# Optimization experiments

Hardware: AMD Instinct MI355X
Metric: run time of the kernel (lower is better)

Reference implementation:

```python
import jax, jax.numpy as jnp
import numpy as np

B, N, D = 4, 4096, 1024


def setup_inputs() -> dict:
    key = jax.random.key(0)
    ks = jax.random.split(key, 7)
    s = 1.0 / np.sqrt(D)
    return {
        "x": jax.random.normal(ks[0], (B, N, D), dtype=jnp.float32),
        "Wq": jax.random.uniform(ks[1], (D, D), jnp.float32, -s, s),
        "bq": jax.random.uniform(ks[2], (D,), jnp.float32, -s, s),
        "Wk": jax.random.uniform(ks[3], (D, D), jnp.float32, -s, s),
        "bk": jax.random.uniform(ks[4], (D,), jnp.float32, -s, s),
        "Wv": jax.random.uniform(ks[5], (D, D), jnp.float32, -s, s),
        "bv": jax.random.uniform(ks[6], (D,), jnp.float32, -s, s),
    }


def reference(x, Wq, bq, Wk, bk, Wv, bv):
    # Projections (nn.Linear: x @ W.T + b; here W stored as [in, out])
    Q = x @ Wq + bq
    K = x @ Wk + bk
    V = x @ Wv + bv
    Qp = jax.nn.elu(Q) + 1.0  # positive feature map
    Kp = jax.nn.elu(K) + 1.0
    KV = jnp.einsum('bnd,bne->bde', Kp, V)          # [B, D, D]
    numerator = jnp.einsum('bnd,bde->bne', Qp, KV)  # [B, N, D]
    K_sum = Kp.sum(axis=1)                           # [B, D]
    norm = jnp.einsum('bnd,bd->bn', Qp, K_sum)[..., None]
    eps = 1e-6
    return numerator / (norm + eps)
```

## Files before the change

kernel.cpp:

```cpp
#include <hip/hip_runtime.h>
#include <hip/hip_bf16.h>
#include <cstdint>

typedef __bf16 bf16x8 __attribute__((ext_vector_type(8)));
typedef float  f32x4  __attribute__((ext_vector_type(4)));
typedef unsigned short u16x8 __attribute__((ext_vector_type(8)));

__device__ __forceinline__ unsigned short f2bf(float f) {
  __hip_bfloat16 h = __float2bfloat16(f);
  return __builtin_bit_cast(unsigned short, h);
}
__device__ __forceinline__ float bf2f(unsigned short u) {
  return __builtin_bit_cast(float, (unsigned)u << 16);
}

#define GL2LDS16(gp, lp)                                                      \
  __builtin_amdgcn_global_load_lds(                                           \
      (const __attribute__((address_space(1))) unsigned int*)(gp),            \
      (__attribute__((address_space(3))) unsigned int*)(lp), 16, 0, 0)

#define SBAR                                                                  \
  {                                                                           \
    __builtin_amdgcn_s_barrier();                                             \
    __builtin_amdgcn_sched_barrier(0);                                        \
  }
#define WAITV(n)                                                              \
  {                                                                           \
    asm volatile("s_waitcnt vmcnt(" #n ")" ::: "memory");                     \
    __builtin_amdgcn_sched_barrier(0);                                        \
  }
#define WAITL0                                                                \
  {                                                                           \
    asm volatile("s_waitcnt lgkmcnt(0)" ::: "memory");                        \
    __builtin_amdgcn_sched_barrier(0);                                        \
  }

template <int MODE>
__global__ __launch_bounds__(512, 2) void gemm256(
    const unsigned short* __restrict__ A, long long lda, long long aOffZ,
    const unsigned short* __restrict__ B, long long ldb, long long bOffZ,
    void* __restrict__ C, long long ldc, long long cOffZ,
    const float* __restrict__ bias, const float* __restrict__ bias2,
    const float* __restrict__ norm, long long normOffZ, int K) {
  __shared__ __attribute__((aligned(16))) char lds[4 * 32768];
  const int t = threadIdx.x;
  const int wave = t >> 6, lane = t & 63;
  const int wm = wave >> 2, wn = wave & 3;
  const int fr = lane & 15, fq = lane >> 4;

  const int gx = gridDim.x, gy = gridDim.y;
  int flat = blockIdx.y * gx + blockIdx.x;
  const int total = gx * gy;
  if ((total & 7) == 0) flat = (flat & 7) * (total >> 3) + (flat >> 3);
  int bx, by;
  if (MODE == 1) {
    bx = flat / gy;
    by = flat - bx * gy;
  } else {
    bx = flat % gx;
    by = flat / gx;
  }
  const int m0 = by * 256, n0 = bx * 256;

  const long long z = blockIdx.z;
  long long aBase, bBase;
  if (MODE == 3) {
    const long long koff = (z & 3) * 4096 + (z >> 2) * 1024;
    aBase = koff;
    bBase = koff;
  } else {
    aBase = z * aOffZ;
    bBase = z * bOffZ;
  }
  const unsigned short* Az = A + aBase;
  const unsigned short* Bz = B + bBase;

  const unsigned short* gA[2];
  const unsigned short* gB[2];
#pragma unroll
  for (int c = 0; c < 2; ++c) {
    int d = c * 8192 + t * 16;
    int l = d ^ (((d >> 7) & 3) << 4);
    int row = l >> 6, kel = (l & 63) >> 1;
    gA[c] = Az + (long long)(m0 + row) * lda + kel;
    gB[c] = Bz + (long long)(n0 + row) * ldb + kel;
  }

  const int slotx = (fr >> 1) & 3;
  const int abase = wm * 8192 + fr * 64 + ((fq ^ slotx) << 4);
  const int bbase = 16384 + wn * 4096 + fr * 64 + ((fq ^ slotx) << 4);

  f32x4 acc[8][4];
#pragma unroll
  for (int i = 0; i < 8; ++i)
#pragma unroll
    for (int j = 0; j < 4; ++j) acc[i][j] = (f32x4){0.f, 0.f, 0.f, 0.f};

  const int NT = K >> 5;

  auto stage = [&](int tile) {
    const int k0 = tile << 5;
    char* bufp = lds + (tile & 3) * 32768;
#pragma unroll
    for (int c = 0; c < 2; ++c)
      GL2LDS16(gA[c] + k0, bufp + c * 8192 + wave * 1024);
#pragma unroll
    for (int c = 0; c < 2; ++c)
      GL2LDS16(gB[c] + k0, bufp + 16384 + c * 8192 + wave * 1024);
  };

  stage(0);
  stage(1);
  stage(2);
  WAITV(8);
  SBAR;

  bf16x8 av[8], bv[4];
  for (int tt = 0; tt < NT - 3; ++tt) {
    const char* bufp = lds + (tt & 3) * 32768;
    stage(tt + 3);
#pragma unroll
    for (int i = 0; i < 4; ++i) {
      av[i] = *(const bf16x8*)(bufp + abase + i * 1024);
      av[4 + i] = *(const bf16x8*)(bufp + abase + 4096 + i * 1024);
      bv[i] = *(const bf16x8*)(bufp + bbase + i * 1024);
    }
    WAITL0;
    __builtin_amdgcn_s_setprio(1);
#pragma unroll
    for (int mi = 0; mi < 8; ++mi)
#pragma unroll
      for (int ni = 0; ni < 4; ++ni)
        acc[mi][ni] = __builtin_amdgcn_mfma_f32_16x16x32_bf16(
            av[mi], bv[ni], acc[mi][ni], 0, 0, 0);
    __builtin_amdgcn_s_setprio(0);
    WAITV(8);
    SBAR;
  }

  WAITV(0);
  SBAR;
#pragma unroll
  for (int e = 0; e < 3; ++e) {
    const char* bufp = lds + ((NT - 3 + e) & 3) * 32768;
#pragma unroll
    for (int i = 0; i < 4; ++i) {
      av[i] = *(const bf16x8*)(bufp + abase + i * 1024);
      av[4 + i] = *(const bf16x8*)(bufp + abase + 4096 + i * 1024);
      bv[i] = *(const bf16x8*)(bufp + bbase + i * 1024);
    }
#pragma unroll
    for (int mi = 0; mi < 8; ++mi)
#pragma unroll
      for (int ni = 0; ni < 4; ++ni)
        acc[mi][ni] = __builtin_amdgcn_mfma_f32_16x16x32_bf16(
            av[mi], bv[ni], acc[mi][ni], 0, 0, 0);
  }

  const float* nrmz = (MODE == 4) ? (norm + z * normOffZ) : nullptr;
  float* Cf = (float*)C + z * cOffZ;
  unsigned short* Cu = (unsigned short*)C + z * cOffZ;
  const bool lower = (m0 < 1024);
#pragma unroll
  for (int mi = 0; mi < 8; ++mi) {
    const int rbase = m0 + wm * 128 + mi * 16 + fq * 4;
    float rb[4], nv[4];
#pragma unroll
    for (int j = 0; j < 4; ++j) {
      if (MODE == 1)
        rb[j] = lower ? bias[rbase + j] : bias2[rbase - 1024 + j];
      if (MODE == 4) nv[j] = nrmz[rbase + j];
    }
#pragma unroll
    for (int ni = 0; ni < 4; ++ni) {
      const int c = n0 + wn * 64 + ni * 16 + fr;
      float cb = 0.f;
      if (MODE == 0) cb = bias[c];
#pragma unroll
      for (int j = 0; j < 4; ++j) {
        float v = acc[mi][ni][j];
        if (MODE == 0) v += cb;
        if (MODE == 1) v += rb[j];
        if (MODE == 0 || (MODE == 1 && lower))
          v = (v > 0.f) ? v + 1.f : __expf(v);
        const long long ci = (long long)(rbase + j) * ldc + c;
        if (MODE == 4)
          Cf[ci] = v / nv[j];
        else
          Cu[ci] = f2bf(v);
      }
    }
  }
}

__global__ __launch_bounds__(256) void reduce_kvt(
    const unsigned short* __restrict__ P, unsigned short* __restrict__ KVt) {
  const long long i = ((long long)blockIdx.x * 256 + threadIdx.x) * 8;
  const int b = (int)(i >> 20);
  const long long ed = i & ((1ll << 20) - 1);
  float s[8] = {0.f, 0.f, 0.f, 0.f, 0.f, 0.f, 0.f, 0.f};
#pragma unroll
  for (int ks = 0; ks < 4; ++ks) {
    u16x8 v = *(const u16x8*)(P + ((long long)(ks * 4 + b) << 20) + ed);
#pragma unroll
    for (int j = 0; j < 8; ++j) s[j] += bf2f(v[j]);
  }
  u16x8 o;
#pragma unroll
  for (int j = 0; j < 8; ++j) o[j] = f2bf(s[j]);
  *(u16x8*)(KVt + i) = o;
}

__global__ __launch_bounds__(256) void transpose_w(
    const float* __restrict__ W, unsigned short* __restrict__ WT) {
  __shared__ float tile[32][33];
  const int tx = threadIdx.x & 31, ty = threadIdx.x >> 5;
  const int i0 = blockIdx.y * 32, o0 = blockIdx.x * 32;
#pragma unroll
  for (int s = 0; s < 32; s += 8)
    tile[ty + s][tx] = W[(long long)(i0 + ty + s) * 1024 + o0 + tx];
  __syncthreads();
#pragma unroll
  for (int s = 0; s < 32; s += 8)
    WT[(long long)(o0 + ty + s) * 1024 + i0 + tx] = f2bf(tile[tx][ty + s]);
}

__global__ __launch_bounds__(256) void convert_x(
    const float4* __restrict__ in, uint2* __restrict__ out, int n4) {
  const int stride = gridDim.x * blockDim.x;
  for (int i = blockIdx.x * blockDim.x + threadIdx.x; i < n4; i += stride) {
    float4 v = in[i];
    uint2 o;
    o.x = (unsigned)f2bf(v.x) | ((unsigned)f2bf(v.y) << 16);
    o.y = (unsigned)f2bf(v.z) | ((unsigned)f2bf(v.w) << 16);
    out[i] = o;
  }
}

__global__ __launch_bounds__(256) void ksum_kernel(
    const unsigned short* __restrict__ KpT, float* __restrict__ Ksum) {
  const int gw = (blockIdx.x * 256 + threadIdx.x) >> 6;
  const int lane = threadIdx.x & 63;
  const int d = gw >> 2, b = gw & 3;
  const unsigned short* p = KpT + (long long)d * 16384 + b * 4096 + lane * 8;
  float s = 0.f;
#pragma unroll
  for (int it = 0; it < 8; ++it) {
    u16x8 v = *(const u16x8*)(p + it * 512);
#pragma unroll
    for (int j = 0; j < 8; ++j) s += bf2f(v[j]);
  }
#pragma unroll
  for (int o = 32; o > 0; o >>= 1) s += __shfl_down(s, o, 64);
  if (lane == 0) Ksum[b * 1024 + d] = s;
}

__global__ __launch_bounds__(256) void norm_kernel(
    const unsigned short* __restrict__ Qp, const float* __restrict__ Ksum,
    float* __restrict__ nrm) {
  const int gw = (blockIdx.x * 256 + threadIdx.x) >> 6;
  const int lane = threadIdx.x & 63;
  const int b = gw >> 12;
  const unsigned short* q = Qp + (long long)gw * 1024 + lane * 8;
  const float* ks = Ksum + b * 1024 + lane * 8;
  float s = 0.f;
#pragma unroll
  for (int it = 0; it < 2; ++it) {
    u16x8 v = *(const u16x8*)(q + it * 512);
    float4 k0 = *(const float4*)(ks + it * 512);
    float4 k1 = *(const float4*)(ks + it * 512 + 4);
    s += bf2f(v[0]) * k0.x + bf2f(v[1]) * k0.y + bf2f(v[2]) * k0.z +
         bf2f(v[3]) * k0.w + bf2f(v[4]) * k1.x + bf2f(v[5]) * k1.y +
         bf2f(v[6]) * k1.z + bf2f(v[7]) * k1.w;
  }
#pragma unroll
  for (int o = 32; o > 0; o >>= 1) s += __shfl_down(s, o, 64);
  if (lane == 0) nrm[gw] = s + 1e-6f;
}

extern "C" void kernel_launch(void* const* d_in, const int* in_sizes, int n_in,
                              void* d_out, int out_size, void* d_ws,
                              size_t ws_size, hipStream_t stream) {
  const float* x  = (const float*)d_in[0];
  const float* Wq = (const float*)d_in[1];
  const float* bq = (const float*)d_in[2];
  const float* Wk = (const float*)d_in[3];
  const float* bk = (const float*)d_in[4];
  const float* Wv = (const float*)d_in[5];
  const float* bv = (const float*)d_in[6];
  float* out = (float*)d_out;

  const size_t MN = 16384ull * 1024ull;
  char* w = (char*)d_ws;
  unsigned short* xb  = (unsigned short*)w;  w += MN * 2;
  unsigned short* WT  = (unsigned short*)w;  w += 3ull * 1024 * 1024 * 2;
  unsigned short* Qp  = (unsigned short*)w;  w += MN * 2;
  unsigned short* KVb = (unsigned short*)w;  w += 2 * MN * 2;
  unsigned short* KVt = (unsigned short*)w;  w += 4ull * 1024 * 1024 * 2;
  float* Ksum = (float*)w;  w += 4ull * 1024 * 4;
  float* nrm  = (float*)w;  w += 16384ull * 4;
  unsigned short* Pkv = xb;
  unsigned short* KpT = KVb;
  unsigned short* VT  = KVb + MN;

  transpose_w<<<dim3(32, 32), 256, 0, stream>>>(Wq, WT);
  transpose_w<<<dim3(32, 32), 256, 0, stream>>>(Wk, WT + 1024 * 1024);
  transpose_w<<<dim3(32, 32), 256, 0, stream>>>(Wv, WT + 2 * 1024 * 1024);
  convert_x<<<2048, 256, 0, stream>>>((const float4*)x, (uint2*)xb,
                                      (int)(MN / 4));

  gemm256<0><<<dim3(4, 64, 1), 512, 0, stream>>>(
      xb, 1024, 0, WT, 1024, 0, Qp, 1024, 0, bq, nullptr, nullptr, 0, 1024);
  gemm256<1><<<dim3(64, 8, 1), 512, 0, stream>>>(
      WT + 1024 * 1024, 1024, 0, xb, 1024, 0, KVb, 16384, 0, bk, bv, nullptr,
      0, 1024);
  ksum_kernel<<<1024, 256, 0, stream>>>(KpT, Ksum);
  gemm256<3><<<dim3(4, 4, 16), 512, 0, stream>>>(
      VT, 16384, 0, KpT, 16384, 0, Pkv, 1024, 1024 * 1024, nullptr, nullptr,
      nullptr, 0, 1024);
  reduce_kvt<<<2048, 256, 0, stream>>>(Pkv, KVt);
  norm_kernel<<<4096, 256, 0, stream>>>(Qp, Ksum, nrm);
  gemm256<4><<<dim3(4, 16, 4), 512, 0, stream>>>(
      Qp, 1024, 4096ll * 1024, KVt, 1024, 1024 * 1024, out, 1024,
      4096ll * 1024, nullptr, nullptr, nrm, 4096, 1024);
}
```

Before: 254.8 us.

## Restructure GEMM main loop into double-buffered 64-wide K tiles with sub-stage interleaving

Replaces the 4-deep ring of 32-wide K tiles with two 64 KB buffers, each holding a 64-wide K tile. Each iteration is split into four sub-phases that interleave LDS fragment reads, quarter-tile global-to-LDS prefetches for the next tile, and half-sized MFMA blocks. The aim is to lower register pressure (av shrinks from 8 to 4 vectors) and spread load issue across the compute. In exchange it adds many more barriers per K step and cuts prefetch depth to one tile ahead, which may expose memory latency.

```diff
diff --git a/kernel.cpp b/kernel.cpp
--- a/kernel.cpp
+++ b/kernel.cpp
@@ -42,7 +42,7 @@
     void* __restrict__ C, long long ldc, long long cOffZ,
     const float* __restrict__ bias, const float* __restrict__ bias2,
     const float* __restrict__ norm, long long normOffZ, int K) {
-  __shared__ __attribute__((aligned(16))) char lds[4 * 32768];
+  __shared__ __attribute__((aligned(16))) char lds[2 * 65536];
   const int t = threadIdx.x;
   const int wave = t >> 6, lane = t & 63;
   const int wm = wave >> 2, wn = wave & 3;
@@ -87,8 +87,8 @@
   }
 
   const int slotx = (fr >> 1) & 3;
-  const int abase = wm * 8192 + fr * 64 + ((fq ^ slotx) << 4);
-  const int bbase = 16384 + wn * 4096 + fr * 64 + ((fq ^ slotx) << 4);
+  const int acore = wm * 8192 + fr * 64 + ((fq ^ slotx) << 4);
+  const int bcore = wn * 4096 + fr * 64 + ((fq ^ slotx) << 4);
 
   f32x4 acc[8][4];
 #pragma unroll
@@ -96,65 +96,149 @@
 #pragma unroll
     for (int j = 0; j < 4; ++j) acc[i][j] = (f32x4){0.f, 0.f, 0.f, 0.f};
 
-  const int NT = K >> 5;
-
-  auto stage = [&](int tile) {
-    const int k0 = tile << 5;
-    char* bufp = lds + (tile & 3) * 32768;
-#pragma unroll
-    for (int c = 0; c < 2; ++c)
-      GL2LDS16(gA[c] + k0, bufp + c * 8192 + wave * 1024);
-#pragma unroll
-    for (int c = 0; c < 2; ++c)
-      GL2LDS16(gB[c] + k0, bufp + 16384 + c * 8192 + wave * 1024);
+  const int NT = K >> 6;
+
+  auto stage_sub = [&](int tile, int which) {
+    char* dst = lds + (tile & 1) * 65536 + which * 16384 + wave * 1024;
+    const int kofs = (tile << 6) + ((which >> 1) << 5);
+    if (which & 1) {
+      GL2LDS16(gB[0] + kofs, dst);
+      GL2LDS16(gB[1] + kofs, dst + 8192);
+    } else {
+      GL2LDS16(gA[0] + kofs, dst);
+      GL2LDS16(gA[1] + kofs, dst + 8192);
+    }
   };
 
-  stage(0);
-  stage(1);
-  stage(2);
-  WAITV(8);
+  stage_sub(0, 0);
+  stage_sub(0, 1);
+  stage_sub(0, 2);
+  stage_sub(0, 3);
+  WAITV(4);
   SBAR;
 
-  bf16x8 av[8], bv[4];
-  for (int tt = 0; tt < NT - 3; ++tt) {
-    const char* bufp = lds + (tt & 3) * 32768;
-    stage(tt + 3);
+  bf16x8 av[4], bv0[4], bv1[4];
+  for (int tt = 0; tt < NT - 1; ++tt) {
+    const char* bufp = lds + (tt & 1) * 65536;
 #pragma unroll
     for (int i = 0; i < 4; ++i) {
-      av[i] = *(const bf16x8*)(bufp + abase + i * 1024);
-      av[4 + i] = *(const bf16x8*)(bufp + abase + 4096 + i * 1024);
-      bv[i] = *(const bf16x8*)(bufp + bbase + i * 1024);
-    }
+      av[i] = *(const bf16x8*)(bufp + acore + i * 1024);
+      bv0[i] = *(const bf16x8*)(bufp + 16384 + bcore + i * 1024);
+    }
+    stage_sub(tt + 1, 0);
+    SBAR;
     WAITL0;
     __builtin_amdgcn_s_setprio(1);
 #pragma unroll
-    for (int mi = 0; mi < 8; ++mi)
+    for (int mi = 0; mi < 4; ++mi)
 #pragma unroll
       for (int ni = 0; ni < 4; ++ni)
         acc[mi][ni] = __builtin_amdgcn_mfma_f32_16x16x32_bf16(
-            av[mi], bv[ni], acc[mi][ni], 0, 0, 0);
+            av[mi], bv0[ni], acc[mi][ni], 0, 0, 0);
     __builtin_amdgcn_s_setprio(0);
-    WAITV(8);
-    SBAR;
-  }
-
-  WAITV(0);
-  SBAR;
-#pragma unroll
-  for (int e = 0; e < 3; ++e) {
-    const char* bufp = lds + ((NT - 3 + e) & 3) * 32768;
+    SBAR;
+#pragma unroll
+    for (int i = 0; i < 4; ++i)
+      av[i] = *(const bf16x8*)(bufp + acore + (4 + i) * 1024);
+    stage_sub(tt + 1, 1);
+    SBAR;
+    WAITL0;
+    __builtin_amdgcn_s_setprio(1);
+#pragma unroll
+    for (int mi = 0; mi < 4; ++mi)
+#pragma unroll
+      for (int ni = 0; ni < 4; ++ni)
+        acc[4 + mi][ni] = __builtin_amdgcn_mfma_f32_16x16x32_bf16(
+            av[mi], bv0[ni], acc[4 + mi][ni], 0, 0, 0);
+    __builtin_amdgcn_s_setprio(0);
+    WAITV(4);
+    SBAR;
 #pragma unroll
     for (int i = 0; i < 4; ++i) {
-      av[i] = *(const bf16x8*)(bufp + abase + i * 1024);
-      av[4 + i] = *(const bf16x8*)(bufp + abase + 4096 + i * 1024);
-      bv[i] = *(const bf16x8*)(bufp + bbase + i * 1024);
-    }
-#pragma unroll
-    for (int mi = 0; mi < 8; ++mi)
+      av[i] = *(const bf16x8*)(bufp + 32768 + acore + i * 1024);
+      bv1[i] = *(const bf16x8*)(bufp + 49152 + bcore + i * 1024);
+    }
+    stage_sub(tt + 1, 2);
+    SBAR;
+    WAITL0;
+    __builtin_amdgcn_s_setprio(1);
+#pragma unroll
+    for (int mi = 0; mi < 4; ++mi)
 #pragma unroll
       for (int ni = 0; ni < 4; ++ni)
         acc[mi][ni] = __builtin_amdgcn_mfma_f32_16x16x32_bf16(
-            av[mi], bv[ni], acc[mi][ni], 0, 0, 0);
+            av[mi], bv1[ni], acc[mi][ni], 0, 0, 0);
+    __builtin_amdgcn_s_setprio(0);
+    SBAR;
+#pragma unroll
+    for (int i = 0; i < 4; ++i)
+      av[i] = *(const bf16x8*)(bufp + 32768 + acore + (4 + i) * 1024);
+    stage_sub(tt + 1, 3);
+    SBAR;
+    WAITL0;
+    __builtin_amdgcn_s_setprio(1);
+#pragma unroll
+    for (int mi = 0; mi < 4; ++mi)
+#pragma unroll
+      for (int ni = 0; ni < 4; ++ni)
+        acc[4 + mi][ni] = __builtin_amdgcn_mfma_f32_16x16x32_bf16(
+            av[mi], bv1[ni], acc[4 + mi][ni], 0, 0, 0);
+    __builtin_amdgcn_s_setprio(0);
+    WAITV(4);
+    SBAR;
+  }
+
+  {
+    const char* bufp = lds + ((NT - 1) & 1) * 65536;
+#pragma unroll
+    for (int i = 0; i < 4; ++i) {
+      av[i] = *(const bf16x8*)(bufp + acore + i * 1024);
+      bv0[i] = *(const bf16x8*)(bufp + 16384 + bcore + i * 1024);
+    }
+    SBAR;
+    WAITL0;
+#pragma unroll
+    for (int mi = 0; mi < 4; ++mi)
+#pragma unroll
+      for (int ni = 0; ni < 4; ++ni)
+        acc[mi][ni] = __builtin_amdgcn_mfma_f32_16x16x32_bf16(
+            av[mi], bv0[ni], acc[mi][ni], 0, 0, 0);
+    SBAR;
+#pragma unroll
+    for (int i = 0; i < 4; ++i)
+      av[i] = *(const bf16x8*)(bufp + acore + (4 + i) * 1024);
+    SBAR;
+    WAITL0;
+#pragma unroll
+    for (int mi = 0; mi < 4; ++mi)
+#pragma unroll
+      for (int ni = 0; ni < 4; ++ni)
+        acc[4 + mi][ni] = __builtin_amdgcn_mfma_f32_16x16x32_bf16(
+            av[mi], bv0[ni], acc[4 + mi][ni], 0, 0, 0);
+    WAITV(0);
+    SBAR;
+#pragma unroll
+    for (int i = 0; i < 4; ++i) {
+      av[i] = *(const bf16x8*)(bufp + 32768 + acore + i * 1024);
+      bv1[i] = *(const bf16x8*)(bufp + 49152 + bcore + i * 1024);
+    }
+    WAITL0;
+#pragma unroll
+    for (int mi = 0; mi < 4; ++mi)
+#pragma unroll
+      for (int ni = 0; ni < 4; ++ni)
+        acc[mi][ni] = __builtin_amdgcn_mfma_f32_16x16x32_bf16(
+            av[mi], bv1[ni], acc[mi][ni], 0, 0, 0);
+#pragma unroll
+    for (int i = 0; i < 4; ++i)
+      av[i] = *(const bf16x8*)(bufp + 32768 + acore + (4 + i) * 1024);
+    WAITL0;
+#pragma unroll
+    for (int mi = 0; mi < 4; ++mi)
+#pragma unroll
+      for (int ni = 0; ni < 4; ++ni)
+        acc[4 + mi][ni] = __builtin_amdgcn_mfma_f32_16x16x32_bf16(
+            av[mi], bv1[ni], acc[4 + mi][ni], 0, 0, 0);
   }
 
   const float* nrmz = (MODE == 4) ? (norm + z * normOffZ) : nullptr;
```

Measured after the change: 250.9 us. About the same (-1.5%).

## Use 1024-thread blocks with 16 waves and triple-buffered LDS in GEMMs

Applied to the files above, without the earlier changes.

The GEMM kernel now launches 1024 threads (16 waves in a 4x4 grid), and each wave computes a 64x64 sub-tile instead of 128x64. The block tile stays 256x256. Per-wave accumulators and A fragments are halved, each thread issues one global-to-LDS load per operand, and the LDS pipeline drops from 4 stages to 3 (96 KB). The aim is more waves in flight per CU to hide latency, at the cost of less register reuse per LDS read and a shallower prefetch depth.

```diff
diff --git a/kernel.cpp b/kernel.cpp
--- a/kernel.cpp
+++ b/kernel.cpp
@@ -36,13 +36,13 @@
   }
 
 template <int MODE>
-__global__ __launch_bounds__(512, 2) void gemm256(
+__global__ __launch_bounds__(1024, 4) void gemm256w(
     const unsigned short* __restrict__ A, long long lda, long long aOffZ,
     const unsigned short* __restrict__ B, long long ldb, long long bOffZ,
     void* __restrict__ C, long long ldc, long long cOffZ,
     const float* __restrict__ bias, const float* __restrict__ bias2,
     const float* __restrict__ norm, long long normOffZ, int K) {
-  __shared__ __attribute__((aligned(16))) char lds[4 * 32768];
+  __shared__ __attribute__((aligned(16))) char lds[3 * 32768];
   const int t = threadIdx.x;
   const int wave = t >> 6, lane = t & 63;
   const int wm = wave >> 2, wn = wave & 3;
@@ -75,82 +75,89 @@
   const unsigned short* Az = A + aBase;
   const unsigned short* Bz = B + bBase;
 
-  const unsigned short* gA[2];
-  const unsigned short* gB[2];
-#pragma unroll
-  for (int c = 0; c < 2; ++c) {
-    int d = c * 8192 + t * 16;
+  const unsigned short* gA;
+  const unsigned short* gB;
+  {
+    int d = t * 16;
     int l = d ^ (((d >> 7) & 3) << 4);
     int row = l >> 6, kel = (l & 63) >> 1;
-    gA[c] = Az + (long long)(m0 + row) * lda + kel;
-    gB[c] = Bz + (long long)(n0 + row) * ldb + kel;
+    gA = Az + (long long)(m0 + row) * lda + kel;
+    gB = Bz + (long long)(n0 + row) * ldb + kel;
   }
 
   const int slotx = (fr >> 1) & 3;
-  const int abase = wm * 8192 + fr * 64 + ((fq ^ slotx) << 4);
-  const int bbase = 16384 + wn * 4096 + fr * 64 + ((fq ^ slotx) << 4);
-
-  f32x4 acc[8][4];
-#pragma unroll
-  for (int i = 0; i < 8; ++i)
+  const int acore = wm * 4096 + fr * 64 + ((fq ^ slotx) << 4);
+  const int bcore = 16384 + wn * 4096 + fr * 64 + ((fq ^ slotx) << 4);
+
+  f32x4 acc[4][4];
+#pragma unroll
+  for (int i = 0; i < 4; ++i)
 #pragma unroll
     for (int j = 0; j < 4; ++j) acc[i][j] = (f32x4){0.f, 0.f, 0.f, 0.f};
 
   const int NT = K >> 5;
 
   auto stage = [&](int tile) {
+    char* sb = lds + (tile % 3) * 32768 + wave * 1024;
     const int k0 = tile << 5;
-    char* bufp = lds + (tile & 3) * 32768;
-#pragma unroll
-    for (int c = 0; c < 2; ++c)
-      GL2LDS16(gA[c] + k0, bufp + c * 8192 + wave * 1024);
-#pragma unroll
-    for (int c = 0; c < 2; ++c)
-      GL2LDS16(gB[c] + k0, bufp + 16384 + c * 8192 + wave * 1024);
+    GL2LDS16(gA + k0, sb);
+    GL2LDS16(gB + k0, sb + 16384);
   };
 
   stage(0);
   stage(1);
-  stage(2);
-  WAITV(8);
+  WAITV(2);
   SBAR;
 
-  bf16x8 av[8], bv[4];
-  for (int tt = 0; tt < NT - 3; ++tt) {
-    const char* bufp = lds + (tt & 3) * 32768;
-    stage(tt + 3);
+  bf16x8 av[4], bv[4];
+  for (int tt = 0; tt < NT - 2; ++tt) {
+    const char* sb = lds + (tt % 3) * 32768;
+    stage(tt + 2);
 #pragma unroll
     for (int i = 0; i < 4; ++i) {
-      av[i] = *(const bf16x8*)(bufp + abase + i * 1024);
-      av[4 + i] = *(const bf16x8*)(bufp + abase + 4096 + i * 1024);
-      bv[i] = *(const bf16x8*)(bufp + bbase + i * 1024);
+      av[i] = *(const bf16x8*)(sb + acore + i * 1024);
+      bv[i] = *(const bf16x8*)(sb + bcore + i * 1024);
     }
     WAITL0;
     __builtin_amdgcn_s_setprio(1);
 #pragma unroll
-    for (int mi = 0; mi < 8; ++mi)
+    for (int mi = 0; mi < 4; ++mi)
 #pragma unroll
       for (int ni = 0; ni < 4; ++ni)
         acc[mi][ni] = __builtin_amdgcn_mfma_f32_16x16x32_bf16(
             av[mi], bv[ni], acc[mi][ni], 0, 0, 0);
     __builtin_amdgcn_s_setprio(0);
-    WAITV(8);
+    WAITV(2);
     SBAR;
   }
 
-  WAITV(0);
-  SBAR;
-#pragma unroll
-  for (int e = 0; e < 3; ++e) {
-    const char* bufp = lds + ((NT - 3 + e) & 3) * 32768;
+  {
+    const char* sb = lds + ((NT - 2) % 3) * 32768;
 #pragma unroll
     for (int i = 0; i < 4; ++i) {
-      av[i] = *(const bf16x8*)(bufp + abase + i * 1024);
-      av[4 + i] = *(const bf16x8*)(bufp + abase + 4096 + i * 1024);
-      bv[i] = *(const bf16x8*)(bufp + bbase + i * 1024);
-    }
-#pragma unroll
-    for (int mi = 0; mi < 8; ++mi)
+      av[i] = *(const bf16x8*)(sb + acore + i * 1024);
+      bv[i] = *(const bf16x8*)(sb + bcore + i * 1024);
+    }
+    WAITL0;
+#pragma unroll
+    for (int mi = 0; mi < 4; ++mi)
+#pragma unroll
+      for (int ni = 0; ni < 4; ++ni)
+        acc[mi][ni] = __builtin_amdgcn_mfma_f32_16x16x32_bf16(
+            av[mi], bv[ni], acc[mi][ni], 0, 0, 0);
+    WAITV(0);
+    SBAR;
+  }
+  {
+    const char* sb = lds + ((NT - 1) % 3) * 32768;
+#pragma unroll
+    for (int i = 0; i < 4; ++i) {
+      av[i] = *(const bf16x8*)(sb + acore + i * 1024);
+      bv[i] = *(const bf16x8*)(sb + bcore + i * 1024);
+    }
+    WAITL0;
+#pragma unroll
+    for (int mi = 0; mi < 4; ++mi)
 #pragma unroll
       for (int ni = 0; ni < 4; ++ni)
         acc[mi][ni] = __builtin_amdgcn_mfma_f32_16x16x32_bf16(
@@ -162,8 +169,8 @@
   unsigned short* Cu = (unsigned short*)C + z * cOffZ;
   const bool lower = (m0 < 1024);
 #pragma unroll
-  for (int mi = 0; mi < 8; ++mi) {
-    const int rbase = m0 + wm * 128 + mi * 16 + fq * 4;
+  for (int mi = 0; mi < 4; ++mi) {
+    const int rbase = m0 + wm * 64 + mi * 16 + fq * 4;
     float rb[4], nv[4];
 #pragma unroll
     for (int j = 0; j < 4; ++j) {
@@ -309,18 +316,18 @@
   convert_x<<<2048, 256, 0, stream>>>((const float4*)x, (uint2*)xb,
                                       (int)(MN / 4));
 
-  gemm256<0><<<dim3(4, 64, 1), 512, 0, stream>>>(
+  gemm256w<0><<<dim3(4, 64, 1), 1024, 0, stream>>>(
       xb, 1024, 0, WT, 1024, 0, Qp, 1024, 0, bq, nullptr, nullptr, 0, 1024);
-  gemm256<1><<<dim3(64, 8, 1), 512, 0, stream>>>(
+  gemm256w<1><<<dim3(64, 8, 1), 1024, 0, stream>>>(
       WT + 1024 * 1024, 1024, 0, xb, 1024, 0, KVb, 16384, 0, bk, bv, nullptr,
       0, 1024);
   ksum_kernel<<<1024, 256, 0, stream>>>(KpT, Ksum);
-  gemm256<3><<<dim3(4, 4, 16), 512, 0, stream>>>(
+  gemm256w<3><<<dim3(4, 4, 16), 1024, 0, stream>>>(
       VT, 16384, 0, KpT, 16384, 0, Pkv, 1024, 1024 * 1024, nullptr, nullptr,
       nullptr, 0, 1024);
   reduce_kvt<<<2048, 256, 0, stream>>>(Pkv, KVt);
   norm_kernel<<<4096, 256, 0, stream>>>(Qp, Ksum, nrm);
-  gemm256<4><<<dim3(4, 16, 4), 512, 0, stream>>>(
+  gemm256w<4><<<dim3(4, 16, 4), 1024, 0, stream>>>(
       Qp, 1024, 4096ll * 1024, KVt, 1024, 1024 * 1024, out, 1024,
       4096ll * 1024, nullptr, nullptr, nrm, 4096, 1024);
 }
```

Result: faster. 244.9 us (-3.9%).
